# Kernel optimization log

Hardware: AMD Instinct MI355X
Metric: run time of the kernel (lower is better)

Reference implementation:

```python
import jax, jax.numpy as jnp
import numpy as np
from jax import lax

B = 256
C1 = 256          # conv1 channels
NUM_CAPS = 32     # primary capsule types
CAP_DIM = 8       # primary capsule dim
NUM_PRIMARY = NUM_CAPS * 6 * 6  # 1152
NUM_OUT = 10
OUT_DIM = 16
NUM_ROUTING = 3


def squash(v):
    # v: (..., d)
    sq = jnp.sum(v * v, axis=-1, keepdims=True)
    scale = sq / (1.0 + sq)
    return scale * v / jnp.sqrt(sq + 1e-8)


def setup_inputs() -> dict:
    key = jax.random.key(0)
    k = jax.random.split(key, 6)
    x = jax.random.normal(k[0], (B, 1, 28, 28), dtype=jnp.float32)
    # kaiming fan_out init for convs
    conv1_w = jax.random.normal(k[1], (C1, 1, 9, 9), dtype=jnp.float32) * np.sqrt(2.0 / (C1 * 81))
    conv1_b = jnp.zeros((C1,), dtype=jnp.float32)
    pc_out = NUM_CAPS * CAP_DIM  # 256
    pc_w = jax.random.normal(k[2], (pc_out, C1, 9, 9), dtype=jnp.float32) * np.sqrt(2.0 / (pc_out * 81))
    pc_b = jnp.zeros((pc_out,), dtype=jnp.float32)
    W_digit = jax.random.normal(k[3], (NUM_PRIMARY, CAP_DIM, NUM_OUT, OUT_DIM), dtype=jnp.float32) * 0.01
    return {"x": x, "conv1_w": conv1_w, "conv1_b": conv1_b,
            "pc_w": pc_w, "pc_b": pc_b, "W_digit": W_digit}


def _conv(x, w, b, stride):
    y = lax.conv_general_dilated(x, w, (stride, stride), 'VALID',
                                 dimension_numbers=('NCHW', 'OIHW', 'NCHW'))
    return y + b[None, :, None, None]


def reference(x, conv1_w, conv1_b, pc_w, pc_b, W_digit):
    # conv1 + ReLU: (B,1,28,28) -> (B,256,20,20)
    h = jax.nn.relu(_conv(x, conv1_w, conv1_b, 1))
    # primary caps conv: -> (B, 256, 6, 6)
    p = _conv(h, pc_w, pc_b, 2)
    bsz, _, oh, ow = p.shape
    # (B, num_caps, cap_dim, H, W) -> (B, num_caps, H, W, cap_dim) -> (B, N, d)
    p = p.reshape(bsz, NUM_CAPS, CAP_DIM, oh, ow)
    p = jnp.transpose(p, (0, 1, 3, 4, 2)).reshape(bsz, NUM_CAPS * oh * ow, CAP_DIM)
    u = squash(p)  # (B, 1152, 8)
    # dynamic routing
    u_hat = jnp.einsum('bid,idjo->bijo', u, W_digit)  # (B, 1152, 10, 16)
    b_logits = jnp.zeros((bsz, NUM_PRIMARY, NUM_OUT, 1), dtype=u_hat.dtype)
    v = None
    for it in range(NUM_ROUTING):
        c = jax.nn.softmax(b_logits, axis=2)
        s = jnp.sum(c * u_hat, axis=1)          # (B, 10, 16)
        v = squash(s)
        if it < NUM_ROUTING - 1:
            agreement = jnp.sum(u_hat * v[:, None, :, :], axis=-1, keepdims=True)
            b_logits = b_logits + agreement
    return v
```

## Files before the change

### kernel.cpp

```cpp
#include <hip/hip_runtime.h>
#include <hip/hip_bf16.h>

#define NI 1152

typedef __attribute__((ext_vector_type(8))) _Float16 f16x8;
typedef __attribute__((ext_vector_type(4))) float f32x4;
typedef __attribute__((ext_vector_type(8))) unsigned short u16x8;
typedef __attribute__((ext_vector_type(4))) unsigned short u16x4;

static const size_t UHAT_OFF = 0;
static const size_t W5_OFF   = 0;
static const size_t H3_OFF   = 10750976UL;
static const size_t WT1_OFF  = 63179776UL;
static const size_t PP_OFF   = 94371840UL;
static const size_t SP_OFF   = 103809024UL;
static const size_t L_OFF    = 127401984UL;
static const size_t V_OFF    = 139198464UL;

__device__ __forceinline__ unsigned short f2bf(float x) {
    unsigned u = __builtin_bit_cast(unsigned, x);
    u += 0x7fffu + ((u >> 16) & 1u);
    return (unsigned short)(u >> 16);
}
__device__ __forceinline__ float bf2f(unsigned short h) {
    return __builtin_bit_cast(float, (unsigned)h << 16);
}
__device__ __forceinline__ void atomAddF(float* p, float v) {
    __hip_atomic_fetch_add(p, v, __ATOMIC_RELAXED, __HIP_MEMORY_SCOPE_AGENT);
}

#define GLD16(gsrc, ldst)                                                      \
    __builtin_amdgcn_global_load_lds(                                          \
        (__attribute__((address_space(1))) const void*)(gsrc),                 \
        (__attribute__((address_space(3))) void*)(ldst), 16, 0, 0)

__global__ __launch_bounds__(256) void k_prep_w(const float* __restrict__ pcw,
                                                _Float16* __restrict__ w5) {
    __shared__ float sl[5184];
    int oc  = blockIdx.x;
    int ic0 = blockIdx.y * 64;
    const float* src = pcw + (size_t)oc * 20736 + (size_t)ic0 * 81;
    for (int j = threadIdx.x; j < 5184; j += 256) sl[j] = src[j];
    __syncthreads();
    int nt = oc >> 7, row = oc & 127;
    for (int t = threadIdx.x; t < 5184; t += 256) {
        int tap = t >> 6, i = t & 63;
        int ic = ic0 + i;
        int ks = ic >> 5, p = (ic >> 3) & 3, icl = ic & 7;
        w5[((size_t)(((tap * 8 + ks) * 2 + nt) * 4 + p) * 128 + row) * 8 + icl] =
            (_Float16)sl[i * 81 + tap];
    }
}

__global__ void k_transpose_w1(const float* __restrict__ w, float* __restrict__ wT) {
    int t = blockIdx.x, oc = threadIdx.x;
    wT[t * 256 + oc] = w[oc * 81 + t];
}

__global__ __launch_bounds__(256) void k_conv1(const float* __restrict__ x,
                                               const float* __restrict__ wT1,
                                               const float* __restrict__ bias,
                                               _Float16* __restrict__ h3) {
    __shared__ _Float16 hs[2][20][256];
    int b  = blockIdx.y;
    int rp = blockIdx.x;
    int oc = threadIdx.x;
    int oy0 = rp * 2;
    const float* xb = x + (size_t)b * 784;
    float bv = bias[oc];
    float acc0[20], acc1[20];
#pragma unroll
    for (int i = 0; i < 20; ++i) { acc0[i] = bv; acc1[i] = bv; }
    for (int ky = 0; ky < 9; ++ky) {
        const float* r0 = xb + (oy0 + ky) * 28;
        const float* r1 = r0 + 28;
        float x0[28], x1[28];
#pragma unroll
        for (int c = 0; c < 28; ++c) { x0[c] = r0[c]; x1[c] = r1[c]; }
#pragma unroll
        for (int kx = 0; kx < 9; ++kx) {
            float w = wT1[(ky * 9 + kx) * 256 + oc];
#pragma unroll
            for (int px = 0; px < 20; ++px) {
                acc0[px] += x0[px + kx] * w;
                acc1[px] += x1[px + kx] * w;
            }
        }
    }
#pragma unroll
    for (int px = 0; px < 20; ++px) {
        hs[0][px][oc] = (_Float16)fmaxf(acc0[px], 0.f);
        hs[1][px][oc] = (_Float16)fmaxf(acc1[px], 0.f);
    }
    __syncthreads();
    for (int cid = threadIdx.x; cid < 1280; cid += 256) {
        int kp = cid & 31;
        int pos = cid >> 5;
        int ry = pos / 20, px2 = pos % 20;
        int ks = kp >> 2, p = kp & 3;
        f16x8 val = *(const f16x8*)&hs[ry][px2][ks * 32 + p * 8];
        _Float16* dst = h3 + ((size_t)((ks * 400 + (oy0 + ry) * 20 + px2) * 4 + p) * 256 + b) * 8;
        *(f16x8*)dst = val;
    }
}

__global__ __launch_bounds__(256, 4) void k_conv2_mfma(
    const _Float16* __restrict__ h3, const _Float16* __restrict__ w5,
    float* __restrict__ pp) {
    __shared__ _Float16 As[8192], Bs[8192];
    const int mt = blockIdx.x, nt = blockIdx.y, ks = blockIdx.z;
    const int pos = mt >> 1, bhalf = mt & 1;
    const int py = pos / 6, px = pos % 6;
    const int l = threadIdx.x & 63;
    const int w = __builtin_amdgcn_readfirstlane((int)(threadIdx.x >> 6));
    const int wm = w >> 1, wn = w & 1;

    f32x4 acc[4][4];
    const f32x4 z = {0.f, 0.f, 0.f, 0.f};
#pragma unroll
    for (int mi = 0; mi < 4; ++mi)
#pragma unroll
        for (int ni = 0; ni < 4; ++ni) acc[mi][ni] = z;

    const int ch = (l >> 4) * 1024;
    const int am = (wm * 64 + (l & 15)) * 8;
    const int bn = (wn * 64 + (l & 15)) * 8;
    const int lds_off = w * 1024 + l * 8;

    for (int it = 0; it < 41; ++it) {
        const int t0 = 2 * it, t1 = t0 + 1;
        const int tA1 = (t1 > 80) ? 80 : t1;
#pragma unroll
        for (int tl = 0; tl < 2; ++tl) {
            const int tap  = tl ? t1 : t0;
            const int tapA = tl ? tA1 : t0;
            const int y = 2 * py + tapA / 9, xx = 2 * px + tapA % 9;
            const _Float16* asrc = h3 + ((size_t)(ks * 400 + y * 20 + xx) * 4 + w) * 2048 +
                                   bhalf * 1024 + l * 8;
            const _Float16* bsrc = w5 + ((size_t)((tap * 8 + ks) * 2 + nt)) * 4096 + lds_off;
            GLD16(asrc,       As + tl * 4096 + lds_off);
            GLD16(asrc + 512, As + tl * 4096 + lds_off + 512);
            GLD16(bsrc,       Bs + tl * 4096 + lds_off);
            GLD16(bsrc + 512, Bs + tl * 4096 + lds_off + 512);
        }
        __syncthreads();
#pragma unroll
        for (int s = 0; s < 2; ++s) {
            const int pb = s * 4096 + ch;
            f16x8 a[4], b[4];
#pragma unroll
            for (int i = 0; i < 4; ++i) {
                a[i] = *(const f16x8*)(As + pb + am + i * 128);
                b[i] = *(const f16x8*)(Bs + pb + bn + i * 128);
            }
#pragma unroll
            for (int mi = 0; mi < 4; ++mi)
#pragma unroll
                for (int ni = 0; ni < 4; ++ni)
                    acc[mi][ni] = __builtin_amdgcn_mfma_f32_16x16x32_f16(a[mi], b[ni], acc[mi][ni], 0, 0, 0);
        }
        __syncthreads();
    }
    const int row0 = (l >> 4) * 4;
    const int ncol = l & 15;
#pragma unroll
    for (int mi = 0; mi < 4; ++mi)
#pragma unroll
        for (int ni = 0; ni < 4; ++ni) {
            int n = nt * 128 + wn * 64 + ni * 16 + ncol;
#pragma unroll
            for (int reg = 0; reg < 4; ++reg) {
                int m = pos * 256 + bhalf * 128 + wm * 64 + mi * 16 + row0 + reg;
                atomAddF(&pp[(size_t)m * 256 + n], acc[mi][ni][reg]);
            }
        }
}

__global__ __launch_bounds__(256) void k_postconv(const float* __restrict__ pp,
                                                  const float* __restrict__ bias,
                                                  const float* __restrict__ W,
                                                  unsigned short* __restrict__ UH,
                                                  float* __restrict__ SP) {
    int it = blockIdx.x, bt = blockIdx.y;
    int i0 = it * 8, b0 = bt * 64;
    int og = threadIdx.x & 3, b_l = threadIdx.x >> 2;
    int b = b0 + b_l;
    float acc[10][4];
#pragma unroll
    for (int j = 0; j < 10; ++j)
#pragma unroll
        for (int o = 0; o < 4; ++o) acc[j][o] = 0.f;
#pragma unroll
    for (int li = 0; li < 8; ++li) {
        int i = i0 + li;
        int cap = i / 36, posi = i - cap * 36;
        const float* p0 = pp + ((size_t)posi * 256 + b) * 256 + cap * 8;
        float4 pa = ((const float4*)p0)[0];
        float4 pb = ((const float4*)p0)[1];
        const float* bs = bias + cap * 8;
        float s8[8] = {pa.x + bs[0], pa.y + bs[1], pa.z + bs[2], pa.w + bs[3],
                       pb.x + bs[4], pb.y + bs[5], pb.z + bs[6], pb.w + bs[7]};
        float sq = 0.f;
#pragma unroll
        for (int d = 0; d < 8; ++d) sq += s8[d] * s8[d];
        float scale = sq / ((1.0f + sq) * sqrtf(sq + 1e-8f));
        float u8[8];
#pragma unroll
        for (int d = 0; d < 8; ++d) u8[d] = scale * s8[d];
        const float* Wi = W + (size_t)i * 1280 + og * 4;
#pragma unroll
        for (int j = 0; j < 10; ++j) {
            float o4[4] = {0.f, 0.f, 0.f, 0.f};
#pragma unroll
            for (int d = 0; d < 8; ++d) {
                float4 wv = *(const float4*)(Wi + d * 160 + j * 16);
                o4[0] += u8[d] * wv.x; o4[1] += u8[d] * wv.y;
                o4[2] += u8[d] * wv.z; o4[3] += u8[d] * wv.w;
            }
            u16x4 h;
#pragma unroll
            for (int o = 0; o < 4; ++o) { h[o] = f2bf(o4[o]); acc[j][o] += o4[o]; }
            *(u16x4*)(UH + ((size_t)(i * 10 + j) * 256 + b) * 16 + og * 4) = h;
        }
    }
    float* sp = SP + ((size_t)it * 256 + b) * 160 + og * 4;
#pragma unroll
    for (int j = 0; j < 10; ++j)
        *(float4*)(sp + j * 16) = make_float4(0.1f * acc[j][0], 0.1f * acc[j][1],
                                              0.1f * acc[j][2], 0.1f * acc[j][3]);
}

__global__ __launch_bounds__(256) void k_route_as(float* __restrict__ L,
                                                  const unsigned short* __restrict__ UH,
                                                  const float* __restrict__ V,
                                                  float* __restrict__ SP,
                                                  int add, int storeL) {
    __shared__ float VL[64][165];
    __shared__ float LG[64][81];
    int it = blockIdx.x, bt = blockIdx.y;
    int b0 = bt * 64, i0 = it * 8;
    int b_l = threadIdx.x & 63;
    int ig = __builtin_amdgcn_readfirstlane((int)(threadIdx.x >> 6));
    int b_r = threadIdx.x >> 2, part = threadIdx.x & 3;
    {
        const float4* vsrc = (const float4*)(V + (size_t)(b0 + b_r) * 160 + part * 40);
#pragma unroll
        for (int q = 0; q < 10; ++q) {
            float4 vv = vsrc[q]; int c = part * 40 + q * 4;
            VL[b_r][c] = vv.x; VL[b_r][c + 1] = vv.y; VL[b_r][c + 2] = vv.z; VL[b_r][c + 3] = vv.w;
        }
        if (add) {
            const float4* lsrc = (const float4*)(L + (size_t)(b0 + b_r) * 11520 + i0 * 10 + part * 20);
#pragma unroll
            for (int q = 0; q < 5; ++q) {
                float4 t = lsrc[q]; int c = part * 20 + q * 4;
                LG[b_r][c] = t.x; LG[b_r][c + 1] = t.y; LG[b_r][c + 2] = t.z; LG[b_r][c + 3] = t.w;
            }
        }
    }
    __syncthreads();
#pragma unroll
    for (int ii = 0; ii < 2; ++ii) {
        int il = ig * 2 + ii;
        int i = i0 + il;
        const unsigned short* up = UH + ((size_t)i * 10 * 256 + b0 + b_l) * 16;
#pragma unroll
        for (int j = 0; j < 10; ++j) {
            u16x8 ua = *(const u16x8*)(up + j * 4096);
            u16x8 ub = *(const u16x8*)(up + j * 4096 + 8);
            float a = 0.f;
#pragma unroll
            for (int o = 0; o < 8; ++o) a += bf2f(ua[o]) * VL[b_l][j * 16 + o];
#pragma unroll
            for (int o = 0; o < 8; ++o) a += bf2f(ub[o]) * VL[b_l][j * 16 + 8 + o];
            float base = add ? LG[b_l][il * 10 + j] : 0.f;
            LG[b_l][il * 10 + j] = base + a;
        }
    }
    __syncthreads();
    if (storeL) {
        float4* ldst = (float4*)(L + (size_t)(b0 + b_r) * 11520 + i0 * 10 + part * 20);
#pragma unroll
        for (int q = 0; q < 5; ++q) {
            int c = part * 20 + q * 4;
            ldst[q] = make_float4(LG[b_r][c], LG[b_r][c + 1], LG[b_r][c + 2], LG[b_r][c + 3]);
        }
    }
    float acc[10][4];
#pragma unroll
    for (int j = 0; j < 10; ++j)
#pragma unroll
        for (int o = 0; o < 4; ++o) acc[j][o] = 0.f;
    for (int li = 0; li < 8; ++li) {
        float lg[10];
#pragma unroll
        for (int j = 0; j < 10; ++j) lg[j] = LG[b_l][li * 10 + j];
        float m = lg[0];
#pragma unroll
        for (int j = 1; j < 10; ++j) m = fmaxf(m, lg[j]);
        float e[10], ssum = 0.f;
#pragma unroll
        for (int j = 0; j < 10; ++j) { e[j] = __expf(lg[j] - m); ssum += e[j]; }
        float inv = 1.0f / ssum;
        const unsigned short* up = UH + ((size_t)(i0 + li) * 10 * 256 + b0 + b_l) * 16 + ig * 4;
#pragma unroll
        for (int j = 0; j < 10; ++j) {
            float cj = e[j] * inv;
            u16x4 t = *(const u16x4*)(up + j * 4096);
#pragma unroll
            for (int o = 0; o < 4; ++o) acc[j][o] += cj * bf2f(t[o]);
        }
    }
    float* sp = SP + ((size_t)it * 256 + b0 + b_l) * 160 + ig * 4;
#pragma unroll
    for (int j = 0; j < 10; ++j)
        *(float4*)(sp + j * 16) = make_float4(acc[j][0], acc[j][1], acc[j][2], acc[j][3]);
}

__global__ __launch_bounds__(256) void k_route_v(const float* __restrict__ SP,
                                                 float* __restrict__ vout) {
    int n = blockIdx.x * 256 + threadIdx.x;
    float ssum = 0.f;
    for (int t = 0; t < 144; ++t) ssum += SP[(size_t)t * 40960 + n];
    float sq = ssum * ssum;
    float tot = sq;
#pragma unroll
    for (int mask = 1; mask < 16; mask <<= 1) tot += __shfl_xor(tot, mask, 64);
    float scale = tot / ((1.0f + tot) * sqrtf(tot + 1e-8f));
    vout[n] = scale * ssum;
}

extern "C" void kernel_launch(void* const* d_in, const int* in_sizes, int n_in,
                              void* d_out, int out_size, void* d_ws, size_t ws_size,
                              hipStream_t stream) {
    (void)in_sizes; (void)n_in; (void)out_size; (void)ws_size;
    const float* x   = (const float*)d_in[0];
    const float* c1w = (const float*)d_in[1];
    const float* c1b = (const float*)d_in[2];
    const float* pcw = (const float*)d_in[3];
    const float* pcb = (const float*)d_in[4];
    const float* Wd  = (const float*)d_in[5];
    float* out = (float*)d_out;
    char* wsb  = (char*)d_ws;

    unsigned short* uh = (unsigned short*)(wsb + UHAT_OFF);
    _Float16* w5 = (_Float16*)(wsb + W5_OFF);
    _Float16* h3 = (_Float16*)(wsb + H3_OFF);
    float* wT1 = (float*)(wsb + WT1_OFF);
    float* pp  = (float*)(wsb + PP_OFF);
    float* sp  = (float*)(wsb + SP_OFF);
    float* lg  = (float*)(wsb + L_OFF);
    float* v   = (float*)(wsb + V_OFF);

    hipMemsetAsync(pp, 0, (size_t)9216 * 256 * sizeof(float), stream);
    hipMemsetAsync(w5 + (size_t)81 * 65536, 0, (size_t)65536 * sizeof(_Float16), stream);

    k_prep_w<<<dim3(256, 4), 256, 0, stream>>>(pcw, w5);
    k_transpose_w1<<<81, 256, 0, stream>>>(c1w, wT1);
    k_conv1<<<dim3(10, 256), 256, 0, stream>>>(x, wT1, c1b, h3);
    k_conv2_mfma<<<dim3(72, 2, 8), 256, 0, stream>>>(h3, w5, pp);
    k_postconv<<<dim3(144, 4), 256, 0, stream>>>(pp, pcb, Wd, uh, sp);

    k_route_v<<<160, 256, 0, stream>>>(sp, v);
    k_route_as<<<dim3(144, 4), 256, 0, stream>>>(lg, uh, v, sp, 0, 1);
    k_route_v<<<160, 256, 0, stream>>>(sp, v);
    k_route_as<<<dim3(144, 4), 256, 0, stream>>>(lg, uh, v, sp, 1, 0);
    k_route_v<<<160, 256, 0, stream>>>(sp, out);
}
```

Before: 477.2 us.

## Widen conv2 MFMA tile to full N, fold memsets into weight prep

The primary-caps conv kernel now uses 512-thread blocks covering all 256 output channels, so each A tile (activations) is loaded once instead of once per N half, halving A traffic and block count. Weight prep writes packed 8-element f16 vectors and also zeroes the split-K accumulator and padding tap, replacing two memset calls. Conv1 reuses the previous input row in registers via ping-pong instead of reloading two rows per ky. The larger block raises register and LDS pressure per block, which may lower occupancy.

New measurement: 947.9 us. +98.7%, slower.

```diff
diff --git a/kernel.cpp b/kernel.cpp
--- a/kernel.cpp
+++ b/kernel.cpp
@@ -35,20 +35,33 @@
         (__attribute__((address_space(3))) void*)(ldst), 16, 0, 0)
 
 __global__ __launch_bounds__(256) void k_prep_w(const float* __restrict__ pcw,
-                                                _Float16* __restrict__ w5) {
+                                                _Float16* __restrict__ w5,
+                                                float* __restrict__ pp) {
     __shared__ float sl[5184];
     int oc  = blockIdx.x;
-    int ic0 = blockIdx.y * 64;
-    const float* src = pcw + (size_t)oc * 20736 + (size_t)ic0 * 81;
+    int icb = blockIdx.y;
+    int flat = blockIdx.x * 4 + blockIdx.y;
+    {
+        float* ppz = pp + (size_t)flat * 2304;
+        for (int k = threadIdx.x; k < 2304; k += 256) ppz[k] = 0.f;
+    }
+    if (threadIdx.x < 64)
+        w5[(size_t)81 * 65536 + (size_t)flat * 64 + threadIdx.x] = (_Float16)0.f;
+
+    const float* src = pcw + (size_t)oc * 20736 + (size_t)icb * 64 * 81;
     for (int j = threadIdx.x; j < 5184; j += 256) sl[j] = src[j];
     __syncthreads();
     int nt = oc >> 7, row = oc & 127;
-    for (int t = threadIdx.x; t < 5184; t += 256) {
-        int tap = t >> 6, i = t & 63;
-        int ic = ic0 + i;
-        int ks = ic >> 5, p = (ic >> 3) & 3, icl = ic & 7;
-        w5[((size_t)(((tap * 8 + ks) * 2 + nt) * 4 + p) * 128 + row) * 8 + icl] =
-            (_Float16)sl[i * 81 + tap];
+    for (int c = threadIdx.x; c < 648; c += 256) {
+        int tap = c >> 3, kp = c & 7;
+        int ksl = kp >> 2, p = kp & 3;
+        int ks = icb * 2 + ksl;
+        f16x8 val;
+#pragma unroll
+        for (int icl = 0; icl < 8; ++icl)
+            val[icl] = (_Float16)sl[(ksl * 32 + p * 8 + icl) * 81 + tap];
+        _Float16* dst = w5 + (size_t)tap * 65536 + ks * 8192 + nt * 4096 + p * 1024 + row * 8;
+        *(f16x8*)dst = val;
     }
 }
 
@@ -71,19 +84,23 @@
     float acc0[20], acc1[20];
 #pragma unroll
     for (int i = 0; i < 20; ++i) { acc0[i] = bv; acc1[i] = bv; }
+    float r0[28], r1[28];
+#pragma unroll
+    for (int c = 0; c < 28; ++c) r0[c] = xb[oy0 * 28 + c];
+#pragma unroll
     for (int ky = 0; ky < 9; ++ky) {
-        const float* r0 = xb + (oy0 + ky) * 28;
-        const float* r1 = r0 + 28;
-        float x0[28], x1[28];
-#pragma unroll
-        for (int c = 0; c < 28; ++c) { x0[c] = r0[c]; x1[c] = r1[c]; }
+        float* rA = (ky & 1) ? r1 : r0;
+        float* rB = (ky & 1) ? r0 : r1;
+        const float* rsrc = xb + (oy0 + ky + 1) * 28;
+#pragma unroll
+        for (int c = 0; c < 28; ++c) rB[c] = rsrc[c];
 #pragma unroll
         for (int kx = 0; kx < 9; ++kx) {
             float w = wT1[(ky * 9 + kx) * 256 + oc];
 #pragma unroll
             for (int px = 0; px < 20; ++px) {
-                acc0[px] += x0[px + kx] * w;
-                acc1[px] += x1[px + kx] * w;
+                acc0[px] += rA[px + kx] * w;
+                acc1[px] += rB[px + kx] * w;
             }
         }
     }
@@ -104,16 +121,17 @@
     }
 }
 
-__global__ __launch_bounds__(256, 4) void k_conv2_mfma(
+__global__ __launch_bounds__(512, 6) void k_conv2_mfma(
     const _Float16* __restrict__ h3, const _Float16* __restrict__ w5,
     float* __restrict__ pp) {
-    __shared__ _Float16 As[8192], Bs[8192];
-    const int mt = blockIdx.x, nt = blockIdx.y, ks = blockIdx.z;
+    __shared__ _Float16 As[8192], Bs[16384];
+    const int mt = blockIdx.x, ks = blockIdx.z;
     const int pos = mt >> 1, bhalf = mt & 1;
     const int py = pos / 6, px = pos % 6;
     const int l = threadIdx.x & 63;
     const int w = __builtin_amdgcn_readfirstlane((int)(threadIdx.x >> 6));
-    const int wm = w >> 1, wn = w & 1;
+    const int wm = w >> 2, wn = w & 3;
+    const int kch = l >> 4, fr = l & 15;
 
     f32x4 acc[4][4];
     const f32x4 z = {0.f, 0.f, 0.f, 0.f};
@@ -122,36 +140,38 @@
 #pragma unroll
         for (int ni = 0; ni < 4; ++ni) acc[mi][ni] = z;
 
-    const int ch = (l >> 4) * 1024;
-    const int am = (wm * 64 + (l & 15)) * 8;
-    const int bn = (wn * 64 + (l & 15)) * 8;
-    const int lds_off = w * 1024 + l * 8;
+    const int tlA = w >> 2;
+    const int pA  = w & 3;
 
     for (int it = 0; it < 41; ++it) {
         const int t0 = 2 * it, t1 = t0 + 1;
         const int tA1 = (t1 > 80) ? 80 : t1;
+        {
+            const int tapA = tlA ? tA1 : t0;
+            const int y = 2 * py + tapA / 9, xx = 2 * px + tapA % 9;
+            const _Float16* asrc = h3 + ((size_t)(ks * 400 + y * 20 + xx) * 4 + pA) * 2048 +
+                                   bhalf * 1024 + l * 8;
+            GLD16(asrc,       As + tlA * 4096 + pA * 1024 + l * 8);
+            GLD16(asrc + 512, As + tlA * 4096 + pA * 1024 + l * 8 + 512);
+        }
 #pragma unroll
         for (int tl = 0; tl < 2; ++tl) {
-            const int tap  = tl ? t1 : t0;
-            const int tapA = tl ? tA1 : t0;
-            const int y = 2 * py + tapA / 9, xx = 2 * px + tapA % 9;
-            const _Float16* asrc = h3 + ((size_t)(ks * 400 + y * 20 + xx) * 4 + w) * 2048 +
-                                   bhalf * 1024 + l * 8;
-            const _Float16* bsrc = w5 + ((size_t)((tap * 8 + ks) * 2 + nt)) * 4096 + lds_off;
-            GLD16(asrc,       As + tl * 4096 + lds_off);
-            GLD16(asrc + 512, As + tl * 4096 + lds_off + 512);
-            GLD16(bsrc,       Bs + tl * 4096 + lds_off);
-            GLD16(bsrc + 512, Bs + tl * 4096 + lds_off + 512);
+            const int tap = tl ? t1 : t0;
+            const _Float16* bsrc = w5 + ((size_t)(tap * 8 + ks)) * 8192 + w * 1024 + l * 8;
+            GLD16(bsrc,       Bs + tl * 8192 + w * 1024 + l * 8);
+            GLD16(bsrc + 512, Bs + tl * 8192 + w * 1024 + l * 8 + 512);
         }
         __syncthreads();
 #pragma unroll
-        for (int s = 0; s < 2; ++s) {
-            const int pb = s * 4096 + ch;
+        for (int tl = 0; tl < 2; ++tl) {
+            const _Float16* Ab = As + tl * 4096 + kch * 1024 + (wm * 64 + fr) * 8;
+            const _Float16* Bb = Bs + tl * 8192 + (wn >> 1) * 4096 + kch * 1024 +
+                                 ((wn & 1) * 64 + fr) * 8;
             f16x8 a[4], b[4];
 #pragma unroll
             for (int i = 0; i < 4; ++i) {
-                a[i] = *(const f16x8*)(As + pb + am + i * 128);
-                b[i] = *(const f16x8*)(Bs + pb + bn + i * 128);
+                a[i] = *(const f16x8*)(Ab + i * 128);
+                b[i] = *(const f16x8*)(Bb + i * 128);
             }
 #pragma unroll
             for (int mi = 0; mi < 4; ++mi)
@@ -161,13 +181,12 @@
         }
         __syncthreads();
     }
-    const int row0 = (l >> 4) * 4;
-    const int ncol = l & 15;
+    const int row0 = kch * 4;
 #pragma unroll
     for (int mi = 0; mi < 4; ++mi)
 #pragma unroll
         for (int ni = 0; ni < 4; ++ni) {
-            int n = nt * 128 + wn * 64 + ni * 16 + ncol;
+            int n = wn * 64 + ni * 16 + fr;
 #pragma unroll
             for (int reg = 0; reg < 4; ++reg) {
                 int m = pos * 256 + bhalf * 128 + wm * 64 + mi * 16 + row0 + reg;
@@ -352,13 +371,10 @@
     float* lg  = (float*)(wsb + L_OFF);
     float* v   = (float*)(wsb + V_OFF);
 
-    hipMemsetAsync(pp, 0, (size_t)9216 * 256 * sizeof(float), stream);
-    hipMemsetAsync(w5 + (size_t)81 * 65536, 0, (size_t)65536 * sizeof(_Float16), stream);
-
-    k_prep_w<<<dim3(256, 4), 256, 0, stream>>>(pcw, w5);
+    k_prep_w<<<dim3(256, 4), 256, 0, stream>>>(pcw, w5, pp);
     k_transpose_w1<<<81, 256, 0, stream>>>(c1w, wT1);
     k_conv1<<<dim3(10, 256), 256, 0, stream>>>(x, wT1, c1b, h3);
-    k_conv2_mfma<<<dim3(72, 2, 8), 256, 0, stream>>>(h3, w5, pp);
+    k_conv2_mfma<<<dim3(72, 1, 8), 512, 0, stream>>>(h3, w5, pp);
     k_postconv<<<dim3(144, 4), 256, 0, stream>>>(pp, pcb, Wd, uh, sp);
 
     k_route_v<<<160, 256, 0, stream>>>(sp, v);
```
